# Kernel tuning notes

Hardware: AMD Instinct MI355X
Metric: run time of the kernel (lower is better)

## Reference

```python
import jax, jax.numpy as jnp
import numpy as np

TAU_MEM = 10.0
TAU_SYN = 5.0
REFRACTORY = 2.0
THRESHOLD = 1.0
TRACE_DECAY = 0.95


def setup_inputs() -> dict:
    key = jax.random.key(0)
    k1, k2, k3 = jax.random.split(key, 3)
    T, D, N = 1000, 64, 128
    return {
        "input_signal": jax.random.normal(k1, (T, D), dtype=jnp.float32),
        "input_weights": jax.random.normal(k2, (D, N), dtype=jnp.float32) * 0.1,
        "recurrent_weights": jax.random.normal(k3, (N, N), dtype=jnp.float32) * 0.05,
        "n_timesteps": 1000,
    }


def reference(input_signal, input_weights, recurrent_weights, n_timesteps):
    # Faithful to the torch code: batch_size = input_signal.shape[0] (= T here),
    # and each timestep's input current (1, N) broadcasts across all B rows.
    B = input_signal.shape[0]
    N = input_weights.shape[1]
    dtype = input_signal.dtype
    # Precompute per-step input currents (T, N); valid since n_timesteps == T.
    inp_cur = input_signal[:n_timesteps] @ input_weights

    def step(state, x_t):
        mem, syn, trace, refr = state
        rec = trace @ recurrent_weights                      # (B, N)
        syn = syn * (1.0 - 1.0 / TAU_SYN) + x_t[None, :] + rec
        mem = mem * (1.0 - 1.0 / TAU_MEM) + syn / TAU_MEM
        mem = jnp.where(refr > 0, jnp.zeros_like(mem), mem)  # refractory masking
        refr = jnp.maximum(refr - 1.0, 0.0)
        spikes = (mem > THRESHOLD).astype(dtype)
        mem = mem * (1.0 - spikes)                           # reset on spike
        refr = refr + spikes * REFRACTORY
        trace = trace * TRACE_DECAY + spikes
        return (mem, syn, trace, refr), (spikes, mem)

    z = jnp.zeros((B, N), dtype)
    (_, _, trace, _), (spk, memh) = jax.lax.scan(step, (z, z, z, z), inp_cur)
    spike_trains = jnp.transpose(spk, (1, 0, 2))       # (B, T, N)
    membrane_history = jnp.transpose(memh, (1, 0, 2))  # (B, T, N)
    return spike_trains, membrane_history, trace
```

## Files before the change

### kernel.cpp

```cpp
#include <hip/hip_runtime.h>
#include <math.h>


#define XCHUNK 8

typedef float vf4 __attribute__((ext_vector_type(4)));

__global__ void inpcur_kernel(const float* __restrict__ sig,
                              const float* __restrict__ win,
                              double* __restrict__ inp_cur,
                              int D, int N) {
    const int t = blockIdx.x;
    const int n = threadIdx.x;
    const float* srow = sig + (size_t)t * D;
    double acc = 0.0;
    for (int d = 0; d < D; ++d)
        acc += (double)srow[d] * (double)win[(size_t)d * N + n];
    inp_cur[(size_t)t * N + n] = acc;
}

__global__ __launch_bounds__(64, 1) void sim_kernel(
    const double* __restrict__ inp_cur,
    const float* __restrict__ wrec,
    float* __restrict__ spk_out,
    float* __restrict__ mem_out,
    float* __restrict__ trace_out,
    int nt) {
    __shared__ float lds_w[128 * 128];

    const int l = threadIdx.x;

    __builtin_amdgcn_s_setprio(3);

    {
        const vf4* src = (const vf4*)wrec;
        vf4* dst = (vf4*)lds_w;
        for (int i = 0; i < 64; ++i)
            dst[i * 64 + l] = src[i * 64 + l];
    }

    double mem_lo = 0.0, syn_lo = 0.0, trc_lo = 0.0, refr_lo = 0.0, rec_lo = 0.0;
    double mem_hi = 0.0, syn_hi = 0.0, trc_hi = 0.0, refr_hi = 0.0, rec_hi = 0.0;

    double x_lo[XCHUNK], x_hi[XCHUNK];

    for (int t0 = 0; t0 < nt; t0 += XCHUNK) {
        const int cs = (nt - t0 < XCHUNK) ? (nt - t0) : XCHUNK;
        #pragma unroll
        for (int s = 0; s < XCHUNK; ++s) {
            if (s < cs) {
                x_lo[s] = inp_cur[(size_t)(t0 + s) * 128 + l];
                x_hi[s] = inp_cur[(size_t)(t0 + s) * 128 + l + 64];
            }
        }

        #pragma unroll
        for (int s = 0; s < XCHUNK; ++s) {
            if (s >= cs) break;
            const int t = t0 + s;

            syn_lo = syn_lo * (1.0 - 1.0 / 5.0) + x_lo[s] + rec_lo;
            mem_lo = mem_lo * (1.0 - 1.0 / 10.0) + syn_lo / 10.0;
            if (refr_lo > 0.0) mem_lo = 0.0;
            refr_lo = refr_lo - 1.0;
            if (refr_lo < 0.0) refr_lo = 0.0;
            const bool sp_lo = mem_lo > 1.0;

            syn_hi = syn_hi * (1.0 - 1.0 / 5.0) + x_hi[s] + rec_hi;
            mem_hi = mem_hi * (1.0 - 1.0 / 10.0) + syn_hi / 10.0;
            if (refr_hi > 0.0) mem_hi = 0.0;
            refr_hi = refr_hi - 1.0;
            if (refr_hi < 0.0) refr_hi = 0.0;
            const bool sp_hi = mem_hi > 1.0;

            const unsigned long long m0 = __ballot(sp_lo);
            const unsigned long long m1 = __ballot(sp_hi);

            if (sp_lo) { mem_lo = 0.0; refr_lo += 2.0; }
            trc_lo = trc_lo * 0.95 + (sp_lo ? 1.0 : 0.0);
            if (sp_hi) { mem_hi = 0.0; refr_hi += 2.0; }
            trc_hi = trc_hi * 0.95 + (sp_hi ? 1.0 : 0.0);

            spk_out[(size_t)t * 128 + l]      = sp_lo ? 1.0f : 0.0f;
            spk_out[(size_t)t * 128 + l + 64] = sp_hi ? 1.0f : 0.0f;
            mem_out[(size_t)t * 128 + l]      = (float)mem_lo;
            mem_out[(size_t)t * 128 + l + 64] = (float)mem_hi;

            double add_lo = 0.0, add_hi = 0.0;
            #pragma unroll 1
            for (int half = 0; half < 2; ++half) {
                unsigned long long m = half ? m1 : m0;
                const float* wb = lds_w + (half ? (64 * 128) : 0);
                while (m) {
                    int kk[8];
                    bool vv[8];
                    #pragma unroll
                    for (int j = 0; j < 8; ++j) {
                        vv[j] = (m != 0ull);
                        kk[j] = m ? (int)__builtin_ctzll(m) : 0;
                        m &= (m - 1ull);
                    }
                    float wl[8], wh[8];
                    #pragma unroll
                    for (int j = 0; j < 8; ++j) {
                        wl[j] = wb[kk[j] * 128 + l];
                        wh[j] = wb[kk[j] * 128 + l + 64];
                    }
                    #pragma unroll
                    for (int j = 0; j < 8; ++j) {
                        add_lo += vv[j] ? (double)wl[j] : 0.0;
                        add_hi += vv[j] ? (double)wh[j] : 0.0;
                    }
                }
            }
            rec_lo = rec_lo * 0.95 + add_lo;
            rec_hi = rec_hi * 0.95 + add_hi;
        }
    }
    trace_out[l]      = (float)trc_lo;
    trace_out[l + 64] = (float)trc_hi;
}

__global__ void bcast_kernel(float* __restrict__ out,
                             int TN4, long long TN, long long B_TN) {
    const long long b = (long long)blockIdx.y + 1;
    const int base = blockIdx.x * (blockDim.x * 4) + threadIdx.x;
    const vf4* s0 = (const vf4*)out;
    const vf4* m0 = (const vf4*)(out + B_TN);
    vf4* sd = (vf4*)(out + b * TN);
    vf4* md = (vf4*)(out + B_TN + b * TN);
    #pragma unroll
    for (int j = 0; j < 4; ++j) {
        const int i = base + j * blockDim.x;
        if (i < TN4) {
            __builtin_nontemporal_store(s0[i], &sd[i]);
            __builtin_nontemporal_store(m0[i], &md[i]);
        }
    }
}

__global__ void trace_bcast_kernel(float* __restrict__ tr, int B, int N4) {
    const int idx = blockIdx.x * blockDim.x + threadIdx.x;
    const int total = (B - 1) * N4;
    if (idx >= total) return;
    const int b = idx / N4 + 1;
    const int j = idx - (b - 1) * N4;
    const vf4 v = ((const vf4*)tr)[j];
    __builtin_nontemporal_store(v, &((vf4*)(tr + (size_t)b * N4 * 4))[j]);
}

extern "C" void kernel_launch(void* const* d_in, const int* in_sizes, int n_in,
                              void* d_out, int out_size, void* d_ws, size_t ws_size,
                              hipStream_t stream) {
    const float* sig  = (const float*)d_in[0];
    const float* win  = (const float*)d_in[1];
    const float* wrec = (const float*)d_in[2];

    int N = 1;
    while ((long long)N * N < (long long)in_sizes[2]) ++N;
    const int D = in_sizes[1] / N;
    const int B = in_sizes[0] / D;
    const int nt = (int)((((long long)out_size / B) - N) / (2 * N));

    const long long TN   = (long long)nt * N;
    const long long B_TN = (long long)B * TN;

    float* out = (float*)d_out;
    double* inp_cur = (double*)(out + ((size_t)out_size - 2 * (size_t)TN));

    inpcur_kernel<<<nt, N, 0, stream>>>(sig, win, inp_cur, D, N);

    sim_kernel<<<1, 64, 0, stream>>>(inp_cur, wrec,
                                     out,
                                     out + B_TN,
                                     out + 2 * B_TN,
                                     nt);

    const int TN4 = (int)(TN / 4);
    dim3 bgrid((TN4 + 1023) / 1024, B - 1);
    bcast_kernel<<<bgrid, 256, 0, stream>>>(out, TN4, TN, B_TN);

    const int trace_total = (B - 1) * (N / 4);
    trace_bcast_kernel<<<(trace_total + 255) / 256, 256, 0, stream>>>(
        out + 2 * B_TN, B, N / 4);
}
```

Baseline: 2.053 ms.

## Interleave neuron layout, software-pipeline spike weight gathers, and batch broadcast rows

The sim kernel now gives each lane two adjacent neurons (2l, 2l+1), so inputs, outputs and weight rows are read and written as 2-wide vectors. The spike-driven weight gather is merged across both ballots and double-buffered, issuing the next 8 LDS loads before the current 8 are summed with a tree reduction. Input-current prefetch is double-buffered across chunks. The broadcast kernel loads each source vector once and writes it to up to 128 batch rows, instead of reloading it for every row. The tree summation changes the order of the double-precision adds slightly.

```diff
diff --git a/kernel.cpp b/kernel.cpp
--- a/kernel.cpp
+++ b/kernel.cpp
@@ -4,7 +4,9 @@
 
 #define XCHUNK 8
 
-typedef float vf4 __attribute__((ext_vector_type(4)));
+typedef float  vf4 __attribute__((ext_vector_type(4)));
+typedef float  vf2 __attribute__((ext_vector_type(2)));
+typedef double vd2 __attribute__((ext_vector_type(2)));
 
 __global__ void inpcur_kernel(const float* __restrict__ sig,
                               const float* __restrict__ win,
@@ -38,104 +40,144 @@
         for (int i = 0; i < 64; ++i)
             dst[i * 64 + l] = src[i * 64 + l];
     }
-
-    double mem_lo = 0.0, syn_lo = 0.0, trc_lo = 0.0, refr_lo = 0.0, rec_lo = 0.0;
-    double mem_hi = 0.0, syn_hi = 0.0, trc_hi = 0.0, refr_hi = 0.0, rec_hi = 0.0;
-
-    double x_lo[XCHUNK], x_hi[XCHUNK];
-
-    for (int t0 = 0; t0 < nt; t0 += XCHUNK) {
-        const int cs = (nt - t0 < XCHUNK) ? (nt - t0) : XCHUNK;
-        #pragma unroll
-        for (int s = 0; s < XCHUNK; ++s) {
-            if (s < cs) {
-                x_lo[s] = inp_cur[(size_t)(t0 + s) * 128 + l];
-                x_hi[s] = inp_cur[(size_t)(t0 + s) * 128 + l + 64];
+    const vf2* w2 = (const vf2*)lds_w;
+
+    double mem0 = 0.0, syn0 = 0.0, trc0 = 0.0, refr0 = 0.0, rec0 = 0.0;
+    double mem1 = 0.0, syn1 = 0.0, trc1 = 0.0, refr1 = 0.0, rec1 = 0.0;
+
+    vd2 xa[XCHUNK], xb[XCHUNK];
+
+#define LDX(t) (((const vd2*)(inp_cur + (size_t)(t) * 128))[l])
+
+#define POP8(kk, vv)                                                     \
+    do {                                                                 \
+        _Pragma("unroll") for (int j = 0; j < 8; ++j) {                  \
+            vv[j] = (mA | mB) != 0ull;                                   \
+            if (mA)      { kk[j] = 2 * (int)__builtin_ctzll(mA);     mA &= mA - 1ull; } \
+            else if (mB) { kk[j] = 2 * (int)__builtin_ctzll(mB) + 1; mB &= mB - 1ull; } \
+            else kk[j] = 0;                                              \
+        }                                                                \
+    } while (0)
+
+#define ISSUE8(kk, w)                                                    \
+    do {                                                                 \
+        _Pragma("unroll") for (int j = 0; j < 8; ++j)                    \
+            w[j] = w2[kk[j] * 64 + l];                                   \
+    } while (0)
+
+#define CONSUME8(w, vv)                                                  \
+    do {                                                                 \
+        double e0[8], e1[8];                                             \
+        _Pragma("unroll") for (int j = 0; j < 8; ++j) {                  \
+            float f0 = vv[j] ? w[j].x : 0.0f;                            \
+            float f1 = vv[j] ? w[j].y : 0.0f;                            \
+            e0[j] = (double)f0;                                          \
+            e1[j] = (double)f1;                                          \
+        }                                                                \
+        add0 += ((e0[0] + e0[1]) + (e0[2] + e0[3])) +                    \
+                ((e0[4] + e0[5]) + (e0[6] + e0[7]));                     \
+        add1 += ((e1[0] + e1[1]) + (e1[2] + e1[3])) +                    \
+                ((e1[4] + e1[5]) + (e1[6] + e1[7]));                     \
+    } while (0)
+
+    auto STEP = [&](int t, vd2 x) {
+        syn0 = syn0 * (1.0 - 1.0 / 5.0) + x.x + rec0;
+        mem0 = mem0 * (1.0 - 1.0 / 10.0) + syn0 * 0.1;
+        if (refr0 > 0.0) mem0 = 0.0;
+        refr0 = refr0 - 1.0;
+        if (refr0 < 0.0) refr0 = 0.0;
+        const bool sp0 = mem0 > 1.0;
+
+        syn1 = syn1 * (1.0 - 1.0 / 5.0) + x.y + rec1;
+        mem1 = mem1 * (1.0 - 1.0 / 10.0) + syn1 * 0.1;
+        if (refr1 > 0.0) mem1 = 0.0;
+        refr1 = refr1 - 1.0;
+        if (refr1 < 0.0) refr1 = 0.0;
+        const bool sp1 = mem1 > 1.0;
+
+        unsigned long long mA = __ballot(sp0);
+        unsigned long long mB = __ballot(sp1);
+        const bool anysp = (mA | mB) != 0ull;
+
+        if (sp0) { mem0 = 0.0; refr0 += 2.0; }
+        trc0 = trc0 * 0.95 + (sp0 ? 1.0 : 0.0);
+        if (sp1) { mem1 = 0.0; refr1 += 2.0; }
+        trc1 = trc1 * 0.95 + (sp1 ? 1.0 : 0.0);
+
+        double add0 = 0.0, add1 = 0.0;
+        int  kkA[8], kkB[8];
+        bool vvA[8], vvB[8];
+        vf2  wA[8],  wB[8];
+
+        if (anysp) { POP8(kkA, vvA); ISSUE8(kkA, wA); }
+
+        {
+            vf2 sv; sv.x = sp0 ? 1.0f : 0.0f; sv.y = sp1 ? 1.0f : 0.0f;
+            ((vf2*)(spk_out + (size_t)t * 128))[l] = sv;
+            vf2 mv; mv.x = (float)mem0; mv.y = (float)mem1;
+            ((vf2*)(mem_out + (size_t)t * 128))[l] = mv;
+        }
+
+        if (anysp) {
+            for (;;) {
+                const bool moreB = (mA | mB) != 0ull;
+                if (moreB) { POP8(kkB, vvB); ISSUE8(kkB, wB); }
+                CONSUME8(wA, vvA);
+                if (!moreB) break;
+                const bool moreA = (mA | mB) != 0ull;
+                if (moreA) { POP8(kkA, vvA); ISSUE8(kkA, wA); }
+                CONSUME8(wB, vvB);
+                if (!moreA) break;
             }
         }
-
-        #pragma unroll
-        for (int s = 0; s < XCHUNK; ++s) {
-            if (s >= cs) break;
-            const int t = t0 + s;
-
-            syn_lo = syn_lo * (1.0 - 1.0 / 5.0) + x_lo[s] + rec_lo;
-            mem_lo = mem_lo * (1.0 - 1.0 / 10.0) + syn_lo / 10.0;
-            if (refr_lo > 0.0) mem_lo = 0.0;
-            refr_lo = refr_lo - 1.0;
-            if (refr_lo < 0.0) refr_lo = 0.0;
-            const bool sp_lo = mem_lo > 1.0;
-
-            syn_hi = syn_hi * (1.0 - 1.0 / 5.0) + x_hi[s] + rec_hi;
-            mem_hi = mem_hi * (1.0 - 1.0 / 10.0) + syn_hi / 10.0;
-            if (refr_hi > 0.0) mem_hi = 0.0;
-            refr_hi = refr_hi - 1.0;
-            if (refr_hi < 0.0) refr_hi = 0.0;
-            const bool sp_hi = mem_hi > 1.0;
-
-            const unsigned long long m0 = __ballot(sp_lo);
-            const unsigned long long m1 = __ballot(sp_hi);
-
-            if (sp_lo) { mem_lo = 0.0; refr_lo += 2.0; }
-            trc_lo = trc_lo * 0.95 + (sp_lo ? 1.0 : 0.0);
-            if (sp_hi) { mem_hi = 0.0; refr_hi += 2.0; }
-            trc_hi = trc_hi * 0.95 + (sp_hi ? 1.0 : 0.0);
-
-            spk_out[(size_t)t * 128 + l]      = sp_lo ? 1.0f : 0.0f;
-            spk_out[(size_t)t * 128 + l + 64] = sp_hi ? 1.0f : 0.0f;
-            mem_out[(size_t)t * 128 + l]      = (float)mem_lo;
-            mem_out[(size_t)t * 128 + l + 64] = (float)mem_hi;
-
-            double add_lo = 0.0, add_hi = 0.0;
-            #pragma unroll 1
-            for (int half = 0; half < 2; ++half) {
-                unsigned long long m = half ? m1 : m0;
-                const float* wb = lds_w + (half ? (64 * 128) : 0);
-                while (m) {
-                    int kk[8];
-                    bool vv[8];
-                    #pragma unroll
-                    for (int j = 0; j < 8; ++j) {
-                        vv[j] = (m != 0ull);
-                        kk[j] = m ? (int)__builtin_ctzll(m) : 0;
-                        m &= (m - 1ull);
-                    }
-                    float wl[8], wh[8];
-                    #pragma unroll
-                    for (int j = 0; j < 8; ++j) {
-                        wl[j] = wb[kk[j] * 128 + l];
-                        wh[j] = wb[kk[j] * 128 + l + 64];
-                    }
-                    #pragma unroll
-                    for (int j = 0; j < 8; ++j) {
-                        add_lo += vv[j] ? (double)wl[j] : 0.0;
-                        add_hi += vv[j] ? (double)wh[j] : 0.0;
-                    }
-                }
-            }
-            rec_lo = rec_lo * 0.95 + add_lo;
-            rec_hi = rec_hi * 0.95 + add_hi;
-        }
+        rec0 = rec0 * 0.95 + add0;
+        rec1 = rec1 * 0.95 + add1;
+    };
+
+    #pragma unroll
+    for (int s = 0; s < XCHUNK; ++s)
+        if (s < nt) xa[s] = LDX(s);
+
+    for (int t0 = 0; t0 < nt; t0 += 2 * XCHUNK) {
+        #pragma unroll
+        for (int s = 0; s < XCHUNK; ++s)
+            if (t0 + XCHUNK + s < nt) xb[s] = LDX(t0 + XCHUNK + s);
+        #pragma unroll
+        for (int s = 0; s < XCHUNK; ++s)
+            if (t0 + s < nt) STEP(t0 + s, xa[s]);
+        #pragma unroll
+        for (int s = 0; s < XCHUNK; ++s)
+            if (t0 + 2 * XCHUNK + s < nt) xa[s] = LDX(t0 + 2 * XCHUNK + s);
+        #pragma unroll
+        for (int s = 0; s < XCHUNK; ++s)
+            if (t0 + XCHUNK + s < nt) STEP(t0 + XCHUNK + s, xb[s]);
     }
-    trace_out[l]      = (float)trc_lo;
-    trace_out[l + 64] = (float)trc_hi;
-}
+
+    vf2 tv; tv.x = (float)trc0; tv.y = (float)trc1;
+    ((vf2*)trace_out)[l] = tv;
+
+#undef LDX
+#undef POP8
+#undef ISSUE8
+#undef CONSUME8
+}
+
+#define BROWS 128
 
 __global__ void bcast_kernel(float* __restrict__ out,
-                             int TN4, long long TN, long long B_TN) {
-    const long long b = (long long)blockIdx.y + 1;
-    const int base = blockIdx.x * (blockDim.x * 4) + threadIdx.x;
-    const vf4* s0 = (const vf4*)out;
-    const vf4* m0 = (const vf4*)(out + B_TN);
-    vf4* sd = (vf4*)(out + b * TN);
-    vf4* md = (vf4*)(out + B_TN + b * TN);
-    #pragma unroll
-    for (int j = 0; j < 4; ++j) {
-        const int i = base + j * blockDim.x;
-        if (i < TN4) {
-            __builtin_nontemporal_store(s0[i], &sd[i]);
-            __builtin_nontemporal_store(m0[i], &md[i]);
-        }
+                             long long TN4, long long B_TN, int B) {
+    const long long i = (long long)blockIdx.x * blockDim.x + threadIdx.x;
+    if (i >= TN4) return;
+    const vf4 vs = ((const vf4*)out)[i];
+    const vf4 vm = ((const vf4*)(out + B_TN))[i];
+    vf4* dsp = (vf4*)out;
+    vf4* dme = (vf4*)(out + B_TN);
+    const int b0 = 1 + (int)blockIdx.y * BROWS;
+    int b1 = b0 + BROWS;
+    if (b1 > B) b1 = B;
+    for (int b = b0; b < b1; ++b) {
+        __builtin_nontemporal_store(vs, dsp + (long long)b * TN4 + i);
+        __builtin_nontemporal_store(vm, dme + (long long)b * TN4 + i);
     }
 }
 
@@ -176,9 +218,9 @@
                                      out + 2 * B_TN,
                                      nt);
 
-    const int TN4 = (int)(TN / 4);
-    dim3 bgrid((TN4 + 1023) / 1024, B - 1);
-    bcast_kernel<<<bgrid, 256, 0, stream>>>(out, TN4, TN, B_TN);
+    const long long TN4 = TN / 4;
+    dim3 bgrid((unsigned)((TN4 + 255) / 256), (unsigned)((B - 1 + BROWS - 1) / BROWS));
+    bcast_kernel<<<bgrid, 256, 0, stream>>>(out, TN4, B_TN, B);
 
     const int trace_total = (B - 1) * (N / 4);
     trace_bcast_kernel<<<(trace_total + 255) / 256, 256, 0, stream>>>(
```

Measured after the change: 2.280 ms. 1.11x slower.
